# Performance work log

Measured on AMD Instinct MI355X. Metric: run time of the kernel, lower is better.

The kernel has to match this reference:

```python
import jax, jax.numpy as jnp
import numpy as np

NEG_SLOPE = 0.2


def setup_inputs() -> dict:
    key = jax.random.key(0)
    ks = jax.random.split(key, 7)
    N, E, IN, H, D = 100000, 1000000, 256, 4, 32
    feat = jax.random.normal(ks[0], (N, IN), dtype=jnp.float32)
    W_fc = jax.random.normal(ks[1], (H * D, IN), dtype=jnp.float32) * (1.0 / np.sqrt(IN))
    attn_l = jax.random.normal(ks[2], (1, H, D), dtype=jnp.float32) * 0.1
    attn_r = jax.random.normal(ks[3], (1, H, D), dtype=jnp.float32) * 0.1
    bias = jnp.zeros((H * D,), dtype=jnp.float32)
    src = jax.random.randint(ks[4], (E,), 0, N, dtype=jnp.int32)
    dst = jax.random.randint(ks[5], (E,), 0, N, dtype=jnp.int32)
    return {"feat": feat, "W_fc": W_fc, "attn_l": attn_l, "attn_r": attn_r, "bias": bias, "src": src, "dst": dst}


def reference(feat, W_fc, attn_l, attn_r, bias, src, dst):
    N = feat.shape[0]
    H, D = attn_l.shape[1], attn_l.shape[2]
    # fc projection; note: in the non-tuple path the module uses self.fc for
    # BOTH feat_src and feat_src2, so they are identical.
    h = (feat @ W_fc.T).reshape(N, H, D)  # [N,H,D]
    el = jnp.sum(h * attn_l, axis=-1)  # [N,H]
    er = jnpp_sum = jnp.sum(h * attn_r, axis=-1)  # [N,H]
    e = jax.nn.leaky_relu(el[src] + er[dst], NEG_SLOPE)  # [E,H]
    # edge softmax normalized over incoming edges of each dst node
    e_max = jax.ops.segment_max(e, dst, num_segments=N)  # [N,H]
    ex = jnp.exp(e - e_max[dst])
    denom = jax.ops.segment_sum(ex, dst, num_segments=N)  # [N,H]
    a = ex / denom[dst]  # [E,H]
    # attention-weighted aggregation: sum_e a_e * h[src_e] -> dst
    initial_ft = jax.ops.segment_sum(h[src] * a[:, :, None], dst, num_segments=N)
    # second path: u_mul_v then sum to dst (feat_src2 == feat_dst2 == h)
    add_ft = jax.ops.segment_sum(h[src] * h[dst], dst, num_segments=N)
    rst = initial_ft + add_ft + bias.reshape(1, H, D)
    return rst
```

## Files before the change

kernel.cpp:

```cpp
#include <hip/hip_runtime.h>
#include <hip/hip_bf16.h>
#include <hip/hip_fp16.h>
#include <math.h>

#define NEG_SLOPE 0.2f

typedef __attribute__((ext_vector_type(8))) short short8v;
typedef __attribute__((ext_vector_type(4))) float f32x4;

__device__ __forceinline__ float uas(unsigned int u) { return __uint_as_float(u); }

__device__ __forceinline__ unsigned short f2bf(float x) {
    __hip_bfloat16 b = __float2bfloat16(x);
    return *(unsigned short*)&b;
}

#define NPB_SHIFT 8
#define BCAP_SHIFT 13
#define BCAP (1 << BCAP_SHIFT)
#define BIN_EDGES 2048
#define BS_EPT    4
#define GEMM_BLOCKS 512

__global__ void k_prep(const float* __restrict__ W, const float* __restrict__ al,
                       const float* __restrict__ ar, short* __restrict__ wfrag,
                       int* __restrict__ bcur, int NB) {
    int p = blockIdx.x * 256 + threadIdx.x;
    if (p < NB) bcur[p] = p << BCAP_SHIFT;
    if (p >= 144 * 32) return;
    int n = p >> 5, kg = p & 31;
    float v[8];
    if (n < 128) {
        const float* wp = W + (size_t)n * 256 + kg * 8;
        float4 v0 = *(const float4*)wp;
        float4 v1 = *(const float4*)(wp + 4);
        v[0] = v0.x; v[1] = v0.y; v[2] = v0.z; v[3] = v0.w;
        v[4] = v1.x; v[5] = v1.y; v[6] = v1.z; v[7] = v1.w;
    } else if (n < 136) {
        int i = n - 128, hh = i & 3, lr = i >> 2;
        const float* av = lr ? ar : al;
#pragma unroll
        for (int j = 0; j < 8; j++) v[j] = 0.f;
        for (int c = 0; c < 32; c++) {
            float a = av[hh * 32 + c];
            const float* wp = W + (size_t)(hh * 32 + c) * 256 + kg * 8;
#pragma unroll
            for (int j = 0; j < 8; j++) v[j] += a * wp[j];
        }
    } else {
#pragma unroll
        for (int j = 0; j < 8; j++) v[j] = 0.f;
    }
    short s8[8];
#pragma unroll
    for (int j = 0; j < 8; j++) s8[j] = (short)f2bf(v[j]);
    int kstep = kg >> 2, ntile = n >> 4;
    int L     = (kg & 3) * 16 + (n & 15);
    int slot  = kstep * 9 + ntile;
    *(short8v*)&wfrag[(slot * 64 + L) * 8] = *(short8v*)s8;
}

__global__ __launch_bounds__(512, 4) void k_gemm(const float* __restrict__ feat,
                                                 const short* __restrict__ wfrag,
                                                 unsigned short* __restrict__ hb,
                                                 float* __restrict__ el,
                                                 float* __restrict__ er, int N,
                                                 int ntiles) {
    __shared__ short wlds[36864];
    const int t    = threadIdx.x;
    const int lane = t & 63;
    const int wave = t >> 6;
    const int g    = lane >> 4;
    const int c    = lane & 15;

#pragma unroll
    for (int i = 0; i < 9; i++) {
        int p = t + i * 512;
        *(short8v*)&wlds[(size_t)p * 8] = *(const short8v*)&wfrag[(size_t)p * 8];
    }
    __syncthreads();

    for (int tile = blockIdx.x; tile < ntiles; tile += gridDim.x) {
        const int n0  = tile * 128;
        const int row = n0 + wave * 16 + c;
        const int rc  = row < N ? row : N - 1;
        const float* ap = feat + (size_t)rc * 256 + g * 8;

        float4 a4[16];
#pragma unroll
        for (int ks = 0; ks < 8; ks++) {
            a4[2 * ks]     = *(const float4*)(ap + ks * 32);
            a4[2 * ks + 1] = *(const float4*)(ap + ks * 32 + 4);
        }
#pragma unroll
        for (int i = 0; i < 16; i++)
            asm volatile("" :: "v"(a4[i].x), "v"(a4[i].y),
                              "v"(a4[i].z), "v"(a4[i].w));

        f32x4 acc[9];
#pragma unroll
        for (int nt = 0; nt < 9; nt++) acc[nt] = (f32x4){0.f, 0.f, 0.f, 0.f};

#pragma unroll
        for (int ks = 0; ks < 8; ks++) {
            float4 v0 = a4[2 * ks], v1 = a4[2 * ks + 1];
            short s8[8];
            s8[0] = (short)f2bf(v0.x); s8[1] = (short)f2bf(v0.y);
            s8[2] = (short)f2bf(v0.z); s8[3] = (short)f2bf(v0.w);
            s8[4] = (short)f2bf(v1.x); s8[5] = (short)f2bf(v1.y);
            s8[6] = (short)f2bf(v1.z); s8[7] = (short)f2bf(v1.w);
            short8v afrag = *(short8v*)s8;
#pragma unroll
            for (int nt = 0; nt < 9; nt++) {
                short8v b = *(short8v*)&wlds[(((size_t)ks * 9 + nt) * 64 + lane) * 8];
                acc[nt] = __builtin_amdgcn_mfma_f32_16x16x32_bf16(afrag, b, acc[nt], 0, 0, 0);
            }
        }

#pragma unroll
        for (int r = 0; r < 4; r++) {
            int m = n0 + wave * 16 + g * 4 + r;
            if (m < N) {
#pragma unroll
                for (int nt = 0; nt < 8; nt++)
                    hb[(size_t)m * 128 + nt * 16 + c] = f2bf(acc[nt][r]);
                float av = acc[8][r];
                if (c < 4)      el[(size_t)m * 4 + c]       = av;
                else if (c < 8) er[(size_t)m * 4 + (c - 4)] = av;
            }
        }
    }
}

__global__ __launch_bounds__(512) void k_binscatter(const int* __restrict__ src,
                                                    const int* __restrict__ dst,
                                                    int* __restrict__ bcur,
                                                    unsigned int* __restrict__ binned,
                                                    int E, int NB) {
    __shared__ int hist[512];
    __shared__ int scn[512];
    __shared__ int lcur[512];
    __shared__ int gdelta[512];
    __shared__ int ebuf[BIN_EDGES];
    __shared__ int dbuf[BIN_EDGES];
    int t = threadIdx.x;
    hist[t] = 0;
    __syncthreads();
    int wbase = blockIdx.x * BIN_EDGES;
    int base  = wbase + t;
    int ne    = E - wbase; if (ne > BIN_EDGES) ne = BIN_EDGES;
    int sv[BS_EPT], dv[BS_EPT];
#pragma unroll
    for (int k = 0; k < BS_EPT; k++) {
        int idx = base + k * 512;
        if (idx < E) {
            sv[k] = src[idx];
            dv[k] = dst[idx];
            atomicAdd(&hist[dv[k] >> NPB_SHIFT], 1);
        } else {
            dv[k] = -1;
        }
    }
    __syncthreads();
    scn[t] = hist[t];
    __syncthreads();
    for (int off = 1; off < 512; off <<= 1) {
        int v = (t >= off) ? scn[t - off] : 0;
        __syncthreads();
        scn[t] += v;
        __syncthreads();
    }
    if (t < NB) {
        int h  = hist[t];
        int lb = scn[t] - h;
        int g  = h ? atomicAdd(&bcur[t], h) : 0;
        gdelta[t] = g - lb;
        lcur[t]   = lb;
    }
    __syncthreads();
#pragma unroll
    for (int k = 0; k < BS_EPT; k++) {
        if (dv[k] >= 0) {
            int bkt  = dv[k] >> NPB_SHIFT;
            int slot = atomicAdd(&lcur[bkt], 1);
            ebuf[slot] = sv[k];
            dbuf[slot] = dv[k];
        }
    }
    __syncthreads();
    for (int j = t; j < ne; j += 512) {
        int d = dbuf[j];
        binned[j + gdelta[d >> NPB_SHIFT]] =
            (unsigned int)ebuf[j] | ((unsigned int)(d & 255) << 24);
    }
}

__global__ __launch_bounds__(512) void k_csr(const unsigned int* __restrict__ binned,
                                             const int* __restrict__ bcur,
                                             int* __restrict__ startA,
                                             int* __restrict__ deg,
                                             int* __restrict__ src_csr, int N) {
    __shared__ int hist[256];
    __shared__ int scn[256];
    __shared__ int cur[256];
    __shared__ int sbuf[4096];
    int b = blockIdx.x;
    int t = threadIdx.x;
    int base = b << BCAP_SHIFT;
    int cnt  = bcur[b] - base;
    int node0 = b << NPB_SHIFT;
    if (t < 256) hist[t] = 0;
    __syncthreads();
    for (int i = t; i < cnt; i += 512) {
        unsigned int e = binned[base + i];
        atomicAdd(&hist[e >> 24], 1);
    }
    __syncthreads();
    int h = (t < 256) ? hist[t] : 0;
    if (t < 256) scn[t] = h;
    __syncthreads();
    for (int off = 1; off < 256; off <<= 1) {
        int v = (t < 256 && t >= off) ? scn[t - off] : 0;
        __syncthreads();
        if (t < 256) scn[t] += v;
        __syncthreads();
    }
    if (t < 256) {
        int excl  = scn[t] - h;
        int gnode = node0 + t;
        if (gnode < N) { startA[gnode] = base + excl; deg[gnode] = h; }
        cur[t] = excl;
    }
    __syncthreads();
    if (cnt <= 4096) {
        for (int i = t; i < cnt; i += 512) {
            unsigned int e = binned[base + i];
            int p = atomicAdd(&cur[e >> 24], 1);
            sbuf[p] = (int)(e & 0xFFFFFFu);
        }
        __syncthreads();
        for (int i = t; i < cnt; i += 512)
            src_csr[base + i] = sbuf[i];
    } else {
        for (int i = t; i < cnt; i += 512) {
            unsigned int e = binned[base + i];
            int p = atomicAdd(&cur[e >> 24], 1);
            src_csr[base + p] = (int)(e & 0xFFFFFFu);
        }
    }
}

__global__ __launch_bounds__(256) void k_agg(
        const unsigned int* __restrict__ hbu,
        const float* __restrict__ el, const float* __restrict__ er,
        const int* __restrict__ src_csr, const int* __restrict__ start,
        const int* __restrict__ deg,
        const float* __restrict__ bias, float* __restrict__ out, int N) {
    int wid  = blockIdx.x * 4 + (threadIdx.x >> 6);
    int lane = threadIdx.x & 63;
    if (wid >= N) return;
    int beg = __builtin_amdgcn_readfirstlane(start[wid]);
    int dg  = __builtin_amdgcn_readfirstlane(deg[wid]);
    int head = lane >> 4;

    float er_own = er[(unsigned)(wid << 2) + head];
    unsigned int uh = hbu[(unsigned)(wid << 6) + lane];
    float2 bv = ((const float2*)bias)[lane];

    float S1x = 0.f, S1y = 0.f, S2x = 0.f, S2y = 0.f, dd = 0.f;
    int i = 0;
    for (; i + 8 <= dg; i += 8) {
        int b = beg + i;
        int s[8];
#pragma unroll
        for (int k = 0; k < 8; k++) s[k] = src_csr[b + k];
        unsigned int u[8];
#pragma unroll
        for (int k = 0; k < 8; k++) u[k] = hbu[(unsigned)(s[k] << 6) + lane];
        float ev[8];
#pragma unroll
        for (int k = 0; k < 8; k++) ev[k] = el[(unsigned)(s[k] << 2) + head];
#pragma unroll
        for (int k = 0; k < 8; k++) {
            float tt = ev[k] + er_own;
            tt = fmaxf(tt, NEG_SLOPE * tt);
            float w = __expf(tt);
            float x = uas(u[k] << 16), y = uas(u[k] & 0xFFFF0000u);
            S1x += x; S1y += y;
            S2x += w * x; S2y += w * y;
            dd  += w;
        }
    }
    for (; i + 4 <= dg; i += 4) {
        int b = beg + i;
        int s[4];
#pragma unroll
        for (int k = 0; k < 4; k++) s[k] = src_csr[b + k];
        unsigned int u[4];
#pragma unroll
        for (int k = 0; k < 4; k++) u[k] = hbu[(unsigned)(s[k] << 6) + lane];
        float ev[4];
#pragma unroll
        for (int k = 0; k < 4; k++) ev[k] = el[(unsigned)(s[k] << 2) + head];
#pragma unroll
        for (int k = 0; k < 4; k++) {
            float tt = ev[k] + er_own;
            tt = fmaxf(tt, NEG_SLOPE * tt);
            float w = __expf(tt);
            float x = uas(u[k] << 16), y = uas(u[k] & 0xFFFF0000u);
            S1x += x; S1y += y;
            S2x += w * x; S2y += w * y;
            dd  += w;
        }
    }
    for (; i < dg; i++) {
        int s0 = src_csr[beg + i];
        unsigned int u0 = hbu[(unsigned)(s0 << 6) + lane];
        float tt = el[(unsigned)(s0 << 2) + head] + er_own;
        tt = fmaxf(tt, NEG_SLOPE * tt);
        float w0 = __expf(tt);
        float x0 = uas(u0 << 16), y0 = uas(u0 & 0xFFFF0000u);
        S1x += x0; S1y += y0;
        S2x += w0 * x0; S2y += w0 * y0;
        dd  += w0;
    }

    float hvx = uas(uh << 16), hvy = uas(uh & 0xFFFF0000u);
    float inv = dd > 0.f ? 1.f / dd : 0.f;
    float ox = bv.x + hvx * S1x + S2x * inv;
    float oy = bv.y + hvy * S1y + S2y * inv;
    float2 o = {ox, oy};
    ((float2*)(out + (size_t)wid * 128))[lane] = o;
}

extern "C" void kernel_launch(void* const* d_in, const int* in_sizes, int n_in,
                              void* d_out, int out_size, void* d_ws, size_t ws_size,
                              hipStream_t stream) {
    const float* feat = (const float*)d_in[0];
    const float* W_fc = (const float*)d_in[1];
    const float* al   = (const float*)d_in[2];
    const float* ar   = (const float*)d_in[3];
    const float* bias = (const float*)d_in[4];
    const int*   src  = (const int*)d_in[5];
    const int*   dst  = (const int*)d_in[6];
    const int N = in_sizes[0] / 256;
    const int E = in_sizes[5];
    const int NB = (N + 255) >> NPB_SHIFT;

    char* ws = (char*)d_ws;
    size_t off = 0;
    unsigned int* hbu = (unsigned int*)(ws + off); off += (size_t)N * 64 * 4;
    float* el         = (float*)(ws + off); off += (size_t)N * 4 * 4;
    float* er         = (float*)(ws + off); off += (size_t)N * 4 * 4;
    int* startA       = (int*)(ws + off);   off += (size_t)N * 4;
    int* deg          = (int*)(ws + off);   off += (size_t)N * 4;
    int* src_csr      = (int*)(ws + off);   off += (size_t)NB * BCAP * 4;
    unsigned int* binned = (unsigned int*)(ws + off); off += (size_t)NB * BCAP * 4;
    short* wfrag      = (short*)(ws + off); off += (size_t)72 * 64 * 8 * 2;
    int* bcur         = (int*)(ws + off);   off += 2048;

    float* out = (float*)d_out;

    int ntiles = (N + 127) / 128;
    int binWG  = (E + BIN_EDGES - 1) / BIN_EDGES;

    k_prep<<<18, 256, 0, stream>>>(W_fc, al, ar, wfrag, bcur, NB);
    k_gemm<<<GEMM_BLOCKS, 512, 0, stream>>>(feat, wfrag, (unsigned short*)hbu,
                                            el, er, N, ntiles);
    k_binscatter<<<binWG, 512, 0, stream>>>(src, dst, bcur, binned, E, NB);
    k_csr<<<NB, 512, 0, stream>>>(binned, bcur, startA, deg, src_csr, N);
    k_agg<<<(N + 3) / 4, 256, 0, stream>>>(hbu, el, er, src_csr, startA, deg,
                                           bias, out, N);
}
```

Measured before the change: 263.4 us.

## Precompute per-edge attention weights and softmax denominators in CSR build kernel

The CSR construction kernel now computes exp(leaky_relu(el[src]+er[dst])) for all four heads of each edge, stores the weights as bf16 in CSR order, and accumulates per-node softmax denominators in shared memory. The aggregation kernel then reads these precomputed weights and denominators instead of gathering el and recomputing exp per lane. Per-head work that was repeated by 16 lanes is done once per edge. In exchange it adds an extra per-edge array write and read, shared-memory float atomics, and bf16 rounding of the weights.

```diff
diff --git a/kernel.cpp b/kernel.cpp
--- a/kernel.cpp
+++ b/kernel.cpp
@@ -197,19 +197,26 @@
 
 __global__ __launch_bounds__(512) void k_csr(const unsigned int* __restrict__ binned,
                                              const int* __restrict__ bcur,
+                                             const float* __restrict__ el,
+                                             const float* __restrict__ er,
                                              int* __restrict__ startA,
                                              int* __restrict__ deg,
-                                             int* __restrict__ src_csr, int N) {
+                                             int* __restrict__ src_csr,
+                                             unsigned short* __restrict__ aw,
+                                             float* __restrict__ denom4, int N) {
     __shared__ int hist[256];
     __shared__ int scn[256];
     __shared__ int cur[256];
     __shared__ int sbuf[4096];
+    __shared__ unsigned char nbuf[4096];
+    __shared__ float dsum[256][4];
     int b = blockIdx.x;
     int t = threadIdx.x;
     int base = b << BCAP_SHIFT;
     int cnt  = bcur[b] - base;
     int node0 = b << NPB_SHIFT;
     if (t < 256) hist[t] = 0;
+    for (int i = t; i < 1024; i += 512) ((float*)dsum)[i] = 0.f;
     __syncthreads();
     for (int i = t; i < cnt; i += 512) {
         unsigned int e = binned[base + i];
@@ -235,26 +242,66 @@
     if (cnt <= 4096) {
         for (int i = t; i < cnt; i += 512) {
             unsigned int e = binned[base + i];
-            int p = atomicAdd(&cur[e >> 24], 1);
+            int ld = e >> 24;
+            int p  = atomicAdd(&cur[ld], 1);
             sbuf[p] = (int)(e & 0xFFFFFFu);
+            nbuf[p] = (unsigned char)ld;
         }
         __syncthreads();
-        for (int i = t; i < cnt; i += 512)
-            src_csr[base + i] = sbuf[i];
+        for (int i = t; i < cnt; i += 512) {
+            int s  = sbuf[i];
+            int ld = nbuf[i];
+            src_csr[base + i] = s;
+            float4 elv = *(const float4*)&el[(unsigned)s * 4];
+            float4 erv = *(const float4*)&er[(unsigned)(node0 + ld) * 4];
+            float w0 = elv.x + erv.x; w0 = fmaxf(w0, NEG_SLOPE * w0); w0 = __expf(w0);
+            float w1 = elv.y + erv.y; w1 = fmaxf(w1, NEG_SLOPE * w1); w1 = __expf(w1);
+            float w2 = elv.z + erv.z; w2 = fmaxf(w2, NEG_SLOPE * w2); w2 = __expf(w2);
+            float w3 = elv.w + erv.w; w3 = fmaxf(w3, NEG_SLOPE * w3); w3 = __expf(w3);
+            atomicAdd(&dsum[ld][0], w0);
+            atomicAdd(&dsum[ld][1], w1);
+            atomicAdd(&dsum[ld][2], w2);
+            atomicAdd(&dsum[ld][3], w3);
+            unsigned int lo = (unsigned int)f2bf(w0) | ((unsigned int)f2bf(w1) << 16);
+            unsigned int hi = (unsigned int)f2bf(w2) | ((unsigned int)f2bf(w3) << 16);
+            *(uint2*)&aw[(size_t)(base + i) * 4] = make_uint2(lo, hi);
+        }
     } else {
         for (int i = t; i < cnt; i += 512) {
             unsigned int e = binned[base + i];
-            int p = atomicAdd(&cur[e >> 24], 1);
-            src_csr[base + p] = (int)(e & 0xFFFFFFu);
-        }
+            int ld = e >> 24;
+            int s  = (int)(e & 0xFFFFFFu);
+            int p  = atomicAdd(&cur[ld], 1);
+            src_csr[base + p] = s;
+            float4 elv = *(const float4*)&el[(unsigned)s * 4];
+            float4 erv = *(const float4*)&er[(unsigned)(node0 + ld) * 4];
+            float w0 = elv.x + erv.x; w0 = fmaxf(w0, NEG_SLOPE * w0); w0 = __expf(w0);
+            float w1 = elv.y + erv.y; w1 = fmaxf(w1, NEG_SLOPE * w1); w1 = __expf(w1);
+            float w2 = elv.z + erv.z; w2 = fmaxf(w2, NEG_SLOPE * w2); w2 = __expf(w2);
+            float w3 = elv.w + erv.w; w3 = fmaxf(w3, NEG_SLOPE * w3); w3 = __expf(w3);
+            atomicAdd(&dsum[ld][0], w0);
+            atomicAdd(&dsum[ld][1], w1);
+            atomicAdd(&dsum[ld][2], w2);
+            atomicAdd(&dsum[ld][3], w3);
+            unsigned int lo = (unsigned int)f2bf(w0) | ((unsigned int)f2bf(w1) << 16);
+            unsigned int hi = (unsigned int)f2bf(w2) | ((unsigned int)f2bf(w3) << 16);
+            *(uint2*)&aw[(size_t)(base + p) * 4] = make_uint2(lo, hi);
+        }
+    }
+    __syncthreads();
+    if (t < 256) {
+        int gnode = node0 + t;
+        if (gnode < N)
+            *(float4*)&denom4[(unsigned)gnode * 4] =
+                make_float4(dsum[t][0], dsum[t][1], dsum[t][2], dsum[t][3]);
     }
 }
 
 __global__ __launch_bounds__(256) void k_agg(
         const unsigned int* __restrict__ hbu,
-        const float* __restrict__ el, const float* __restrict__ er,
+        const unsigned short* __restrict__ aw,
         const int* __restrict__ src_csr, const int* __restrict__ start,
-        const int* __restrict__ deg,
+        const int* __restrict__ deg, const float* __restrict__ denom4,
         const float* __restrict__ bias, float* __restrict__ out, int N) {
     int wid  = blockIdx.x * 4 + (threadIdx.x >> 6);
     int lane = threadIdx.x & 63;
@@ -263,11 +310,12 @@
     int dg  = __builtin_amdgcn_readfirstlane(deg[wid]);
     int head = lane >> 4;
 
-    float er_own = er[(unsigned)(wid << 2) + head];
+    float dden = denom4[(unsigned)(wid << 2) + head];
+    float inv  = dden > 0.f ? 1.f / dden : 0.f;
     unsigned int uh = hbu[(unsigned)(wid << 6) + lane];
     float2 bv = ((const float2*)bias)[lane];
 
-    float S1x = 0.f, S1y = 0.f, S2x = 0.f, S2y = 0.f, dd = 0.f;
+    float S1x = 0.f, S1y = 0.f, S2x = 0.f, S2y = 0.f;
     int i = 0;
     for (; i + 8 <= dg; i += 8) {
         int b = beg + i;
@@ -277,18 +325,15 @@
         unsigned int u[8];
 #pragma unroll
         for (int k = 0; k < 8; k++) u[k] = hbu[(unsigned)(s[k] << 6) + lane];
-        float ev[8];
-#pragma unroll
-        for (int k = 0; k < 8; k++) ev[k] = el[(unsigned)(s[k] << 2) + head];
+        unsigned short wv[8];
+#pragma unroll
+        for (int k = 0; k < 8; k++) wv[k] = aw[(unsigned)((b + k) << 2) + head];
 #pragma unroll
         for (int k = 0; k < 8; k++) {
-            float tt = ev[k] + er_own;
-            tt = fmaxf(tt, NEG_SLOPE * tt);
-            float w = __expf(tt);
+            float w = uas((unsigned int)wv[k] << 16);
             float x = uas(u[k] << 16), y = uas(u[k] & 0xFFFF0000u);
             S1x += x; S1y += y;
             S2x += w * x; S2y += w * y;
-            dd  += w;
         }
     }
     for (; i + 4 <= dg; i += 4) {
@@ -299,34 +344,28 @@
         unsigned int u[4];
 #pragma unroll
         for (int k = 0; k < 4; k++) u[k] = hbu[(unsigned)(s[k] << 6) + lane];
-        float ev[4];
-#pragma unroll
-        for (int k = 0; k < 4; k++) ev[k] = el[(unsigned)(s[k] << 2) + head];
+        unsigned short wv[4];
+#pragma unroll
+        for (int k = 0; k < 4; k++) wv[k] = aw[(unsigned)((b + k) << 2) + head];
 #pragma unroll
         for (int k = 0; k < 4; k++) {
-            float tt = ev[k] + er_own;
-            tt = fmaxf(tt, NEG_SLOPE * tt);
-            float w = __expf(tt);
+            float w = uas((unsigned int)wv[k] << 16);
             float x = uas(u[k] << 16), y = uas(u[k] & 0xFFFF0000u);
             S1x += x; S1y += y;
             S2x += w * x; S2y += w * y;
-            dd  += w;
         }
     }
     for (; i < dg; i++) {
-        int s0 = src_csr[beg + i];
+        int b = beg + i;
+        int s0 = src_csr[b];
         unsigned int u0 = hbu[(unsigned)(s0 << 6) + lane];
-        float tt = el[(unsigned)(s0 << 2) + head] + er_own;
-        tt = fmaxf(tt, NEG_SLOPE * tt);
-        float w0 = __expf(tt);
+        float w0 = uas((unsigned int)aw[(unsigned)(b << 2) + head] << 16);
         float x0 = uas(u0 << 16), y0 = uas(u0 & 0xFFFF0000u);
         S1x += x0; S1y += y0;
         S2x += w0 * x0; S2y += w0 * y0;
-        dd  += w0;
     }
 
     float hvx = uas(uh << 16), hvy = uas(uh & 0xFFFF0000u);
-    float inv = dd > 0.f ? 1.f / dd : 0.f;
     float ox = bv.x + hvx * S1x + S2x * inv;
     float oy = bv.y + hvy * S1y + S2y * inv;
     float2 o = {ox, oy};
@@ -354,8 +393,10 @@
     float* er         = (float*)(ws + off); off += (size_t)N * 4 * 4;
     int* startA       = (int*)(ws + off);   off += (size_t)N * 4;
     int* deg          = (int*)(ws + off);   off += (size_t)N * 4;
+    float* denom4     = (float*)(ws + off); off += (size_t)N * 4 * 4;
     int* src_csr      = (int*)(ws + off);   off += (size_t)NB * BCAP * 4;
     unsigned int* binned = (unsigned int*)(ws + off); off += (size_t)NB * BCAP * 4;
+    unsigned short* aw = (unsigned short*)(ws + off); off += (size_t)NB * BCAP * 8;
     short* wfrag      = (short*)(ws + off); off += (size_t)72 * 64 * 8 * 2;
     int* bcur         = (int*)(ws + off);   off += 2048;
 
@@ -368,7 +409,8 @@
     k_gemm<<<GEMM_BLOCKS, 512, 0, stream>>>(feat, wfrag, (unsigned short*)hbu,
                                             el, er, N, ntiles);
     k_binscatter<<<binWG, 512, 0, stream>>>(src, dst, bcur, binned, E, NB);
-    k_csr<<<NB, 512, 0, stream>>>(binned, bcur, startA, deg, src_csr, N);
-    k_agg<<<(N + 3) / 4, 256, 0, stream>>>(hbu, el, er, src_csr, startA, deg,
-                                           bias, out, N);
-}
+    k_csr<<<NB, 512, 0, stream>>>(binned, bcur, el, er, startA, deg, src_csr,
+                                  aw, denom4, N);
+    k_agg<<<(N + 3) / 4, 256, 0, stream>>>(hbu, aw, src_csr, startA, deg,
+                                           denom4, bias, out, N);
+}
```

Result: slower. 292.0 us (+10.8%).
